# Performance work log

Measured on AMD Instinct MI355X. Metric: run time of the kernel, lower is better.

## Reference

```python
import jax, jax.numpy as jnp
import numpy as np

IMG_WIDTH = 128


def setup_inputs() -> dict:
    key = jax.random.key(0)
    k1, _ = jax.random.split(key)
    B, C, H, W = 16, 1, 128, IMG_WIDTH
    inp = jax.random.normal(k1, (B, C, H, W), dtype=jnp.float32)
    mask = jnp.ones((B, 1, 1, W), dtype=jnp.float32)  # unused by the module's forward, kept for signature fidelity
    return {"input": inp, "mask": mask}


def reference(input, mask):
    # input: (B, C, H, W); only channel 0 is used, matching input[:, :1, ...]
    B, _, H, W = input.shape
    # RFFT module in the repo: ortho-normalized full 2D FFT -> (real, imag) channels
    k = jnp.fft.fft2(input[:, 0], norm="ortho")  # (B, H, W) complex64
    # separated_masks: one-hot per frequency column -> keep only column i in copy i
    col_onehot = jnp.eye(W, dtype=k.dtype)  # (W_copy, W_freq)
    # repeat k-space W times and zero all but one column per copy: (B, W, H, W)
    masked_k = k[:, None, :, :] * col_onehot[None, :, None, :]
    # IFFT module: ortho-normalized 2D IFFT; forward keeps the real part ([:, 0, ...])
    out = jnp.fft.ifft2(masked_k, norm="ortho").real.astype(input.dtype)
    return out  # (B, img_width, H, W)
```

## Files before the change

kernel.cpp:

```cpp
#include <hip/hip_runtime.h>
#include <math.h>


#define WDIM 128
#define BLK 256

__global__ __launch_bounds__(BLK) void kspace_map_kernel(
    const float* __restrict__ in, float* __restrict__ out) {
    const int bh = blockIdx.x;
    const int b  = bh >> 7;
    const int h  = bh & 127;

    __shared__ float x[WDIM];
    __shared__ float cosT[WDIM];
    __shared__ float sinT[WDIM];
    __shared__ float c[WDIM];
    __shared__ float s[WDIM];
    __shared__ float cpart[BLK];
    __shared__ float spart[BLK];

    const int t = threadIdx.x;

    if (t < WDIM) {
        x[t] = in[(size_t)bh * WDIM + t];
        double ang = (double)t * (M_PI / 64.0);
        cosT[t] = (float)cos(ang);
        sinT[t] = (float)sin(ang);
    }
    __syncthreads();

    {
        const int i    = t & 127;
        const int half = t >> 7;
        const int base = half * 64;
        float cc = 0.f, ss = 0.f;
        int idx = (i * base) & 127;
        #pragma unroll
        for (int k = 0; k < 64; ++k) {
            float xv = x[base + k];
            cc = fmaf(xv, cosT[idx], cc);
            ss = fmaf(xv, sinT[idx], ss);
            idx = (idx + i) & 127;
        }
        cpart[t] = cc;
        spart[t] = ss;
    }
    __syncthreads();
    if (t < WDIM) {
        c[t] = cpart[t] + cpart[t + 128];
        s[t] = spart[t] + spart[t + 128];
    }
    __syncthreads();

    const float invW = 1.0f / (float)WDIM;
    const int wbase = (t & 31) * 4;
    const int ibase = t >> 5;
    float* outp = out + (((size_t)b * WDIM) * WDIM + h) * WDIM;

    #pragma unroll
    for (int ii = 0; ii < 16; ++ii) {
        const int i = ibase + (ii << 3);
        const float ci = c[i] * invW;
        const float si = s[i] * invW;
        const int step = i;
        int idx = (i * wbase) & 127;
        float4 v;
        v.x = fmaf(ci, cosT[idx], si * sinT[idx]); idx = (idx + step) & 127;
        v.y = fmaf(ci, cosT[idx], si * sinT[idx]); idx = (idx + step) & 127;
        v.z = fmaf(ci, cosT[idx], si * sinT[idx]); idx = (idx + step) & 127;
        v.w = fmaf(ci, cosT[idx], si * sinT[idx]);
        *reinterpret_cast<float4*>(outp + (size_t)i * (WDIM * WDIM) + wbase) = v;
    }
}

extern "C" void kernel_launch(void* const* d_in, const int* in_sizes, int n_in,
                              void* d_out, int out_size, void* d_ws, size_t ws_size,
                              hipStream_t stream) {
    const float* in = (const float*)d_in[0];
    float* out = (float*)d_out;
    const int B = 16, H = 128;
    dim3 grid(B * H);
    dim3 block(BLK);
    hipLaunchKernelGGL(kspace_map_kernel, grid, block, 0, stream, in, out);
}
```

Before: 32.15 us.

## Regrid per frequency column with contiguous nontemporal stores and twiddle recurrence

Reassigns each block to one frequency column and a quarter of the rows, so every block writes a contiguous slab of output using nontemporal vector stores. The forward DFT per row is recomputed per frequency with a rotation recurrence and fast intrinsic sin/cos instead of a shared twiddle table. This aims to improve write coalescing and cut shared memory traffic and syncs, at the cost of redundant input reads and some precision loss from the recurrence and fast trig.

```diff
diff --git a/kernel.cpp b/kernel.cpp
--- a/kernel.cpp
+++ b/kernel.cpp
@@ -4,72 +4,96 @@
 
 #define WDIM 128
 #define BLK 256
+#define PI_OVER_64 0.04908738521234052f
+
+typedef float vfloat4 __attribute__((ext_vector_type(4)));
 
 __global__ __launch_bounds__(BLK) void kspace_map_kernel(
     const float* __restrict__ in, float* __restrict__ out) {
-    const int bh = blockIdx.x;
-    const int b  = bh >> 7;
-    const int h  = bh & 127;
+    const int blk = blockIdx.x;
+    const int i   = blk & 127;
+    const int bq  = blk >> 7;
+    const int q   = bq & 3;
+    const int b   = bq >> 2;
 
-    __shared__ float x[WDIM];
-    __shared__ float cosT[WDIM];
-    __shared__ float sinT[WDIM];
-    __shared__ float c[WDIM];
-    __shared__ float s[WDIM];
-    __shared__ float cpart[BLK];
-    __shared__ float spart[BLK];
+    __shared__ float cS[32];
+    __shared__ float sS[32];
 
     const int t = threadIdx.x;
 
-    if (t < WDIM) {
-        x[t] = in[(size_t)bh * WDIM + t];
-        double ang = (double)t * (M_PI / 64.0);
-        cosT[t] = (float)cos(ang);
-        sinT[t] = (float)sin(ang);
-    }
-    __syncthreads();
+    const int hl  = t >> 3;
+    const int seg = t & 7;
+    const int k0  = seg << 4;
+    const int h   = (q << 5) + hl;
+
+    const float stepA = (float)i * PI_OVER_64;
+    const float stC = __cosf(stepA);
+    const float stS = __sinf(stepA);
 
     {
-        const int i    = t & 127;
-        const int half = t >> 7;
-        const int base = half * 64;
-        float cc = 0.f, ss = 0.f;
-        int idx = (i * base) & 127;
+        const float* xr = in + ((size_t)b << 14) + ((size_t)h << 7) + k0;
+        vfloat4 x0 = *(const vfloat4*)(xr + 0);
+        vfloat4 x1 = *(const vfloat4*)(xr + 4);
+        vfloat4 x2 = *(const vfloat4*)(xr + 8);
+        vfloat4 x3 = *(const vfloat4*)(xr + 12);
+
+        const int idx0 = (i * k0) & 127;
+        float C = __cosf((float)idx0 * PI_OVER_64);
+        float S = __sinf((float)idx0 * PI_OVER_64);
+
+        float cc = 0.0f, ss = 0.0f;
+        float xs[16];
+        *reinterpret_cast<vfloat4*>(&xs[0])  = x0;
+        *reinterpret_cast<vfloat4*>(&xs[4])  = x1;
+        *reinterpret_cast<vfloat4*>(&xs[8])  = x2;
+        *reinterpret_cast<vfloat4*>(&xs[12]) = x3;
         #pragma unroll
-        for (int k = 0; k < 64; ++k) {
-            float xv = x[base + k];
-            cc = fmaf(xv, cosT[idx], cc);
-            ss = fmaf(xv, sinT[idx], ss);
-            idx = (idx + i) & 127;
+        for (int k = 0; k < 16; ++k) {
+            const float xv = xs[k];
+            cc = fmaf(xv, C, cc);
+            ss = fmaf(xv, S, ss);
+            const float nC = fmaf(C, stC, -(S * stS));
+            const float nS = fmaf(S, stC,  (C * stS));
+            C = nC; S = nS;
         }
-        cpart[t] = cc;
-        spart[t] = ss;
-    }
-    __syncthreads();
-    if (t < WDIM) {
-        c[t] = cpart[t] + cpart[t + 128];
-        s[t] = spart[t] + spart[t + 128];
+        #pragma unroll
+        for (int m = 1; m <= 4; m <<= 1) {
+            cc += __shfl_xor(cc, m);
+            ss += __shfl_xor(ss, m);
+        }
+        if (seg == 0) { cS[hl] = cc; sS[hl] = ss; }
     }
     __syncthreads();
 
     const float invW = 1.0f / (float)WDIM;
-    const int wbase = (t & 31) * 4;
-    const int ibase = t >> 5;
-    float* outp = out + (((size_t)b * WDIM) * WDIM + h) * WDIM;
+    const int col = t & 31;
+    const int w0  = col << 2;
+    const int r   = t >> 5;
+
+    const int j0 = (i * w0) & 127;
+    const float Cv0 = __cosf((float)j0 * PI_OVER_64);
+    const float Sv0 = __sinf((float)j0 * PI_OVER_64);
+    const float Cv1 = fmaf(Cv0, stC, -(Sv0 * stS));
+    const float Sv1 = fmaf(Sv0, stC,  (Cv0 * stS));
+    const float Cv2 = fmaf(Cv1, stC, -(Sv1 * stS));
+    const float Sv2 = fmaf(Sv1, stC,  (Cv1 * stS));
+    const float Cv3 = fmaf(Cv2, stC, -(Sv2 * stS));
+    const float Sv3 = fmaf(Sv2, stC,  (Cv2 * stS));
+
+    float* op = out + ((size_t)b << 21) + ((size_t)i << 14) + ((size_t)q << 12);
 
     #pragma unroll
-    for (int ii = 0; ii < 16; ++ii) {
-        const int i = ibase + (ii << 3);
-        const float ci = c[i] * invW;
-        const float si = s[i] * invW;
-        const int step = i;
-        int idx = (i * wbase) & 127;
-        float4 v;
-        v.x = fmaf(ci, cosT[idx], si * sinT[idx]); idx = (idx + step) & 127;
-        v.y = fmaf(ci, cosT[idx], si * sinT[idx]); idx = (idx + step) & 127;
-        v.z = fmaf(ci, cosT[idx], si * sinT[idx]); idx = (idx + step) & 127;
-        v.w = fmaf(ci, cosT[idx], si * sinT[idx]);
-        *reinterpret_cast<float4*>(outp + (size_t)i * (WDIM * WDIM) + wbase) = v;
+    for (int ii = 0; ii < 4; ++ii) {
+        const int hp = (ii << 3) + r;
+        const float ci = cS[hp] * invW;
+        const float si = sS[hp] * invW;
+        vfloat4 v;
+        v.x = fmaf(ci, Cv0, si * Sv0);
+        v.y = fmaf(ci, Cv1, si * Sv1);
+        v.z = fmaf(ci, Cv2, si * Sv2);
+        v.w = fmaf(ci, Cv3, si * Sv3);
+        __builtin_nontemporal_store(
+            v, reinterpret_cast<vfloat4*>(op + ((size_t)hp << 7) + w0));
     }
 }
 
@@ -78,8 +102,7 @@
                               hipStream_t stream) {
     const float* in = (const float*)d_in[0];
     float* out = (float*)d_out;
-    const int B = 16, H = 128;
-    dim3 grid(B * H);
+    dim3 grid(16 * 4 * 128);
     dim3 block(BLK);
     hipLaunchKernelGGL(kspace_map_kernel, grid, block, 0, stream, in, out);
 }
```

New measurement: 29.13 us. 9.4% less time.

## Split work across 4096 blocks and replace twiddle tables with rotation recurrences

Applied to the files above, without the earlier changes.

Each block now handles two image rows and a quarter of the frequency columns, which raises the grid from 2048 to 4096 blocks. The row DFT is split four ways per output with wavefront shuffle reductions, so the shared-memory partial-sum pass goes away. The twiddle factors are no longer read from double-precision shared tables; they come from fast __cosf/__sinf seeds and are advanced by complex-rotation recurrences in registers. This removes the double trig and table lookups at the cost of some accumulated floating-point error. Each block also recomputes part of the row transform that it shares with other blocks.

```diff
diff --git a/kernel.cpp b/kernel.cpp
--- a/kernel.cpp
+++ b/kernel.cpp
@@ -4,72 +4,109 @@
 
 #define WDIM 128
 #define BLK 256
+#define PI_OVER_64 0.04908738521234052f
+
+typedef float vfloat4 __attribute__((ext_vector_type(4)));
 
 __global__ __launch_bounds__(BLK) void kspace_map_kernel(
     const float* __restrict__ in, float* __restrict__ out) {
-    const int bh = blockIdx.x;
-    const int b  = bh >> 7;
-    const int h  = bh & 127;
+    const int blk = blockIdx.x;
+    const int q   = blk & 3;
+    const int rp  = blk >> 2;
+    const int bh0 = rp << 1;
+    const int b   = bh0 >> 7;
+    const int h0  = bh0 & 127;
 
-    __shared__ float x[WDIM];
-    __shared__ float cosT[WDIM];
-    __shared__ float sinT[WDIM];
-    __shared__ float c[WDIM];
-    __shared__ float s[WDIM];
-    __shared__ float cpart[BLK];
-    __shared__ float spart[BLK];
+    __shared__ float x2[2][WDIM];
+    __shared__ float cS[2][32];
+    __shared__ float sS[2][32];
 
     const int t = threadIdx.x;
 
-    if (t < WDIM) {
-        x[t] = in[(size_t)bh * WDIM + t];
-        double ang = (double)t * (M_PI / 64.0);
-        cosT[t] = (float)cos(ang);
-        sinT[t] = (float)sin(ang);
+    {
+        const int srow = t >> 7, scol = t & 127;
+        x2[srow][scol] = in[((size_t)bh0 + srow) * WDIM + scol];
     }
+
+    const int seg = t & 3;
+    const int u   = t >> 2;
+    const int row = u >> 5;
+    const int il  = u & 31;
+    const int ig1 = (q << 5) + il;
+    const int k0  = seg << 5;
+
+    const float a0p = (float)((ig1 * k0) & 127) * PI_OVER_64;
+    float C = __cosf(a0p);
+    float S = __sinf(a0p);
+    const float asp = (float)ig1 * PI_OVER_64;
+    const float stC = __cosf(asp);
+    const float stS = __sinf(asp);
+
     __syncthreads();
 
     {
-        const int i    = t & 127;
-        const int half = t >> 7;
-        const int base = half * 64;
         float cc = 0.f, ss = 0.f;
-        int idx = (i * base) & 127;
         #pragma unroll
-        for (int k = 0; k < 64; ++k) {
-            float xv = x[base + k];
-            cc = fmaf(xv, cosT[idx], cc);
-            ss = fmaf(xv, sinT[idx], ss);
-            idx = (idx + i) & 127;
+        for (int k = 0; k < 32; ++k) {
+            const float xv = x2[row][k0 + k];
+            cc = fmaf(xv, C, cc);
+            ss = fmaf(xv, S, ss);
+            const float nC = fmaf(C, stC, -(S * stS));
+            const float nS = fmaf(S, stC,  (C * stS));
+            C = nC; S = nS;
         }
-        cpart[t] = cc;
-        spart[t] = ss;
-    }
-    __syncthreads();
-    if (t < WDIM) {
-        c[t] = cpart[t] + cpart[t + 128];
-        s[t] = spart[t] + spart[t + 128];
+        cc += __shfl_xor(cc, 1); ss += __shfl_xor(ss, 1);
+        cc += __shfl_xor(cc, 2); ss += __shfl_xor(ss, 2);
+        if (seg == 0) { cS[row][il] = cc; sS[row][il] = ss; }
     }
     __syncthreads();
 
     const float invW = 1.0f / (float)WDIM;
-    const int wbase = (t & 31) * 4;
-    const int ibase = t >> 5;
-    float* outp = out + (((size_t)b * WDIM) * WDIM + h) * WDIM;
+    const int lane = t & 63;
+    const int wv   = t >> 6;
+    const int col  = lane & 31;
+    const int hpar = lane >> 5;
+    const int w0   = col << 2;
+    const int il0  = wv << 3;
+    const int ig0  = (q << 5) + il0;
+
+    const float av = (float)((ig0 * w0) & 127) * PI_OVER_64;
+    float Cv = __cosf(av);
+    float Sv = __sinf(av);
+    const float wA = (float)w0 * PI_OVER_64;
+    const float wC = __cosf(wA);
+    const float wS = __sinf(wA);
+    float tC = __cosf((float)ig0 * PI_OVER_64);
+    float tS = __sinf((float)ig0 * PI_OVER_64);
+    const float oC = 0.99879545620517241f;
+    const float oS = 0.049067674327418015f;
+
+    float* op = out + ((size_t)b << 21) + ((size_t)ig0 << 14)
+                    + ((size_t)(h0 + hpar) << 7) + w0;
 
     #pragma unroll
-    for (int ii = 0; ii < 16; ++ii) {
-        const int i = ibase + (ii << 3);
-        const float ci = c[i] * invW;
-        const float si = s[i] * invW;
-        const int step = i;
-        int idx = (i * wbase) & 127;
-        float4 v;
-        v.x = fmaf(ci, cosT[idx], si * sinT[idx]); idx = (idx + step) & 127;
-        v.y = fmaf(ci, cosT[idx], si * sinT[idx]); idx = (idx + step) & 127;
-        v.z = fmaf(ci, cosT[idx], si * sinT[idx]); idx = (idx + step) & 127;
-        v.w = fmaf(ci, cosT[idx], si * sinT[idx]);
-        *reinterpret_cast<float4*>(outp + (size_t)i * (WDIM * WDIM) + wbase) = v;
+    for (int ii = 0; ii < 8; ++ii) {
+        const int ilc = il0 + ii;
+        const float ci = cS[hpar][ilc] * invW;
+        const float si = sS[hpar][ilc] * invW;
+
+        vfloat4 v;
+        v.x = fmaf(ci, Cv, si * Sv);
+        float c1 = fmaf(Cv, tC, -(Sv * tS)), s1 = fmaf(Sv, tC, Cv * tS);
+        v.y = fmaf(ci, c1, si * s1);
+        float c2 = fmaf(c1, tC, -(s1 * tS)), s2 = fmaf(s1, tC, c1 * tS);
+        v.z = fmaf(ci, c2, si * s2);
+        float c3 = fmaf(c2, tC, -(s2 * tS)), s3 = fmaf(s2, tC, c2 * tS);
+        v.w = fmaf(ci, c3, si * s3);
+        *reinterpret_cast<vfloat4*>(op) = v;
+        op += (size_t)1 << 14;
+
+        const float nCv = fmaf(Cv, wC, -(Sv * wS));
+        const float nSv = fmaf(Sv, wC,  (Cv * wS));
+        Cv = nCv; Sv = nSv;
+        const float ntC = fmaf(tC, oC, -(tS * oS));
+        const float ntS = fmaf(tS, oC,  (tC * oS));
+        tC = ntC; tS = ntS;
     }
 }
 
@@ -78,8 +115,7 @@
                               hipStream_t stream) {
     const float* in = (const float*)d_in[0];
     float* out = (float*)d_out;
-    const int B = 16, H = 128;
-    dim3 grid(B * H);
+    dim3 grid(4096);
     dim3 block(BLK);
     hipLaunchKernelGGL(kspace_map_kernel, grid, block, 0, stream, in, out);
 }
```

Result: faster. 27.60 us (-14.2%).
